# Kernel optimization log

Hardware: AMD Instinct MI355X
Metric: run time of the kernel (lower is better)

The kernel has to match this reference:

```python
import jax, jax.numpy as jnp
import numpy as np


def setup_inputs() -> dict:
    key = jax.random.key(0)
    kZ, kQ, kW, kU, kbk = jax.random.split(key, 5)
    B, E, D = 64, 16, 64
    N_ATOMS = 200000
    N_NP = 160000
    N_BK = 20000
    Q_DIM = 64
    Z = jax.random.normal(kZ, (B, E, D), dtype=jnp.float32)
    Q = jax.random.normal(kQ, (B, Q_DIM), dtype=jnp.float32)
    W = jax.random.normal(kW, (N_NP, D), dtype=jnp.float32)
    U = jax.random.normal(kU, (N_NP, Q_DIM), dtype=jnp.float32)
    np_indices = jnp.arange(N_NP, dtype=jnp.int64 if jax.config.jax_enable_x64 else jnp.int32)
    bk_indices = jax.random.randint(kbk, (N_BK,), 0, N_ATOMS, dtype=jnp.int32)
    return {"Z": Z, "Q": Q, "W": W, "U": U,
            "np_indices": np_indices, "bk_indices": bk_indices,
            "n_atoms": N_ATOMS}


def reference(Z, Q, W, U, np_indices, bk_indices, n_atoms):
    # Batched valuation for all neural-predicate atoms at once:
    # vm(Z, Q, atom_i) = sigmoid(sum_{e,d} Z[b,e,d] * W[i,d] + Q[b] . U[i])
    scores = jax.nn.sigmoid(jnp.einsum('bed,nd->bn', Z, W) + Q @ U.T)  # [B, n_np]
    B = Z.shape[0]
    V = jnp.zeros((B, n_atoms), dtype=jnp.float32)
    V = V.at[:, 0].set(1.0)                 # V[:, 0] = 1.0 (true atom)
    V = V.at[:, np_indices].set(scores)     # scatter valuation outputs
    V = V.at[:, bk_indices].add(1.0)        # background knowledge atoms += 1
    return V
```

## Files before the change

kernel.cpp:

```cpp
#include <hip/hip_runtime.h>


typedef _Float16 half8_t __attribute__((ext_vector_type(8)));
typedef float float4_t __attribute__((ext_vector_type(4)));

#define E_DIM 16
#define D_DIM 64
#define QD    64

__device__ inline half8_t pack8(float4_t lo, float4_t hi) {
    half8_t r;
    r[0] = (_Float16)lo[0]; r[1] = (_Float16)lo[1];
    r[2] = (_Float16)lo[2]; r[3] = (_Float16)lo[3];
    r[4] = (_Float16)hi[0]; r[5] = (_Float16)hi[1];
    r[6] = (_Float16)hi[2]; r[7] = (_Float16)hi[3];
    return r;
}

__global__ void prep_kernel(const float* __restrict__ Z, const float* __restrict__ Q,
                            const int* __restrict__ bk, int n_bk,
                            _Float16* __restrict__ Afrag, float* __restrict__ cnt) {
    int blk = blockIdx.x;
    int tid = threadIdx.x;
    if (blk < 32) {
        int t = blk * 256 + tid;
        int b = t >> 7, k = t & 127;
        float v;
        if (k < D_DIM) {
            const float* zp = Z + (size_t)b * E_DIM * D_DIM + k;
            v = 0.f;
            #pragma unroll
            for (int e = 0; e < E_DIM; ++e) v += zp[e * D_DIM];
        } else {
            v = Q[b * QD + (k - D_DIM)];
        }
        int mt = b >> 4, r = b & 15;
        int kq = k >> 5, j = k & 7, quad = (k >> 3) & 3;
        int lane = r + quad * 16;
        Afrag[(((mt * 4 + kq) * 64) + lane) * 8 + j] = (_Float16)v;
    } else if (cnt) {
        int i = (blk - 32) * 256 + tid;
        if (i < n_bk) atomicAdd(&cnt[bk[i]], 1.0f);
    }
}

__global__ __launch_bounds__(256) void main_kernel(
        const float* __restrict__ W, const float* __restrict__ U,
        const _Float16* __restrict__ Afrag, const float* __restrict__ cnt,
        float* __restrict__ V, int n_np, int n_atoms) {
    int tid = threadIdx.x;
    long long nblk = (long long)blockIdx.x * 64;

    if (nblk >= n_np) {
        int row = tid >> 2;
        long long c0 = nblk + (long long)(tid & 3) * 16;
        float4_t* vp = (float4_t*)(V + (size_t)row * n_atoms + c0);
        if (cnt) {
            const float4_t* cp = (const float4_t*)(cnt + c0);
            #pragma unroll
            for (int q = 0; q < 4; ++q) vp[q] = cp[q];
        } else {
            float4_t z = {0.f, 0.f, 0.f, 0.f};
            #pragma unroll
            for (int q = 0; q < 4; ++q) vp[q] = z;
        }
        return;
    }

    int wv = tid >> 6, lane = tid & 63;
    int quad = lane >> 4, l15 = lane & 15;
    long long n0 = nblk + wv * 16;

    const half8_t* Ap = (const half8_t*)Afrag;
    half8_t a[4][4];
    #pragma unroll
    for (int mt = 0; mt < 4; ++mt)
        #pragma unroll
        for (int kq = 0; kq < 4; ++kq)
            a[mt][kq] = Ap[(mt * 4 + kq) * 64 + lane];

    const float* Wr = W + (size_t)(n0 + l15) * D_DIM + quad * 8;
    const float* Ur = U + (size_t)(n0 + l15) * QD + quad * 8;
    float4_t w0 = *(const float4_t*)(Wr);
    float4_t w1 = *(const float4_t*)(Wr + 4);
    float4_t w2 = *(const float4_t*)(Wr + 32);
    float4_t w3 = *(const float4_t*)(Wr + 36);
    float4_t u0 = *(const float4_t*)(Ur);
    float4_t u1 = *(const float4_t*)(Ur + 4);
    float4_t u2 = *(const float4_t*)(Ur + 32);
    float4_t u3 = *(const float4_t*)(Ur + 36);
    half8_t b0 = pack8(w0, w1);
    half8_t b1 = pack8(w2, w3);
    half8_t b2 = pack8(u0, u1);
    half8_t b3 = pack8(u2, u3);

    float4_t acc[4] = {{0.f,0.f,0.f,0.f},{0.f,0.f,0.f,0.f},
                       {0.f,0.f,0.f,0.f},{0.f,0.f,0.f,0.f}};
    #pragma unroll
    for (int mt = 0; mt < 4; ++mt) {
        acc[mt] = __builtin_amdgcn_mfma_f32_16x16x32_f16(a[mt][0], b0, acc[mt], 0, 0, 0);
        acc[mt] = __builtin_amdgcn_mfma_f32_16x16x32_f16(a[mt][1], b1, acc[mt], 0, 0, 0);
        acc[mt] = __builtin_amdgcn_mfma_f32_16x16x32_f16(a[mt][2], b2, acc[mt], 0, 0, 0);
        acc[mt] = __builtin_amdgcn_mfma_f32_16x16x32_f16(a[mt][3], b3, acc[mt], 0, 0, 0);
    }

    float cn = cnt ? cnt[n0 + l15] : 0.f;
    #pragma unroll
    for (int mt = 0; mt < 4; ++mt) {
        #pragma unroll
        for (int r = 0; r < 4; ++r) {
            int row = mt * 16 + quad * 4 + r;
            float s = 1.0f / (1.0f + __expf(-acc[mt][r])) + cn;
            V[(size_t)row * n_atoms + n0 + l15] = s;
        }
    }
}

__global__ void bk_scatter(const int* __restrict__ bk, int n_bk,
                           float* __restrict__ V, int n_atoms) {
    int i = blockIdx.x * 256 + threadIdx.x;
    if (i < n_bk)
        atomicAdd(&V[(size_t)blockIdx.y * n_atoms + bk[i]], 1.0f);
}

extern "C" void kernel_launch(void* const* d_in, const int* in_sizes, int n_in,
                              void* d_out, int out_size, void* d_ws, size_t ws_size,
                              hipStream_t stream) {
    const float* Z = (const float*)d_in[0];
    const float* Q = (const float*)d_in[1];
    const float* W = (const float*)d_in[2];
    const float* U = (const float*)d_in[3];
    const int* bk = (const int*)d_in[5];
    float* V = (float*)d_out;

    int B       = in_sizes[0] / (E_DIM * D_DIM);
    int n_np    = in_sizes[2] / D_DIM;
    int n_bk    = in_sizes[5];
    int n_atoms = out_size / B;

    _Float16* Afrag = (_Float16*)d_ws;
    size_t need = 16384 + (size_t)n_atoms * sizeof(float);
    bool use_cnt = ws_size >= need;
    float* cnt = use_cnt ? (float*)((char*)d_ws + 16384) : nullptr;

    if (use_cnt) {
        hipMemsetAsync(cnt, 0, (size_t)n_atoms * sizeof(float), stream);
        int cnt_blocks = (n_bk + 255) / 256;
        prep_kernel<<<32 + cnt_blocks, 256, 0, stream>>>(Z, Q, bk, n_bk, Afrag, cnt);
    } else {
        prep_kernel<<<32, 256, 0, stream>>>(Z, Q, bk, n_bk, Afrag, nullptr);
    }

    int nb = n_atoms / 64;
    main_kernel<<<nb, 256, 0, stream>>>(W, U, Afrag, cnt, V, n_np, n_atoms);

    if (!use_cnt) {
        dim3 g((n_bk + 255) / 256, B);
        bk_scatter<<<g, 256, 0, stream>>>(bk, n_bk, V, n_atoms);
    }
}
```

Measured before the change: 142.0 us.

## Stage W/U through LDS and transpose outputs for vectorized coalesced stores

W and U tiles are now loaded cooperatively with fully coalesced float4 reads, converted to fp16 and staged in padded shared memory, and each wave then reads its MFMA B fragments from LDS. The accumulators are written transposed into shared memory so every thread can emit float4 stores along the atom dimension instead of scattered 4-byte stores. The tail blocks use the same float4 layout. This adds two extra barriers and LDS traffic in exchange for wider, better-coalesced global reads and writes of the large output matrix.

```diff
diff --git a/kernel.cpp b/kernel.cpp
--- a/kernel.cpp
+++ b/kernel.cpp
@@ -2,20 +2,12 @@
 
 
 typedef _Float16 half8_t __attribute__((ext_vector_type(8)));
+typedef _Float16 half4_t __attribute__((ext_vector_type(4)));
 typedef float float4_t __attribute__((ext_vector_type(4)));
 
 #define E_DIM 16
 #define D_DIM 64
 #define QD    64
-
-__device__ inline half8_t pack8(float4_t lo, float4_t hi) {
-    half8_t r;
-    r[0] = (_Float16)lo[0]; r[1] = (_Float16)lo[1];
-    r[2] = (_Float16)lo[2]; r[3] = (_Float16)lo[3];
-    r[4] = (_Float16)hi[0]; r[5] = (_Float16)hi[1];
-    r[6] = (_Float16)hi[2]; r[7] = (_Float16)hi[3];
-    return r;
-}
 
 __global__ void prep_kernel(const float* __restrict__ Z, const float* __restrict__ Q,
                             const int* __restrict__ bk, int n_bk,
@@ -44,32 +36,35 @@
     }
 }
 
+#define WH_STRIDE 72
+#define ET_STRIDE 68
+
 __global__ __launch_bounds__(256) void main_kernel(
         const float* __restrict__ W, const float* __restrict__ U,
         const _Float16* __restrict__ Afrag, const float* __restrict__ cnt,
         float* __restrict__ V, int n_np, int n_atoms) {
+    __shared__ __align__(16) char smem_raw[2 * 64 * WH_STRIDE * 2];
     int tid = threadIdx.x;
     long long nblk = (long long)blockIdx.x * 64;
+    int c  = tid & 15;
+    int rr = tid >> 4;
 
     if (nblk >= n_np) {
-        int row = tid >> 2;
-        long long c0 = nblk + (long long)(tid & 3) * 16;
-        float4_t* vp = (float4_t*)(V + (size_t)row * n_atoms + c0);
-        if (cnt) {
-            const float4_t* cp = (const float4_t*)(cnt + c0);
-            #pragma unroll
-            for (int q = 0; q < 4; ++q) vp[q] = cp[q];
-        } else {
-            float4_t z = {0.f, 0.f, 0.f, 0.f};
-            #pragma unroll
-            for (int q = 0; q < 4; ++q) vp[q] = z;
+        float4_t cn4 = {0.f, 0.f, 0.f, 0.f};
+        if (cnt) cn4 = *(const float4_t*)(cnt + nblk + 4 * c);
+        #pragma unroll
+        for (int p = 0; p < 4; ++p) {
+            int row = p * 16 + rr;
+            *(float4_t*)(V + (size_t)row * n_atoms + nblk + 4 * c) = cn4;
         }
         return;
     }
 
+    _Float16(*Wh)[WH_STRIDE] = (_Float16(*)[WH_STRIDE])smem_raw;
+    _Float16(*Uh)[WH_STRIDE] = (_Float16(*)[WH_STRIDE])(smem_raw + 64 * WH_STRIDE * 2);
+
     int wv = tid >> 6, lane = tid & 63;
     int quad = lane >> 4, l15 = lane & 15;
-    long long n0 = nblk + wv * 16;
 
     const half8_t* Ap = (const half8_t*)Afrag;
     half8_t a[4][4];
@@ -79,20 +74,26 @@
         for (int kq = 0; kq < 4; ++kq)
             a[mt][kq] = Ap[(mt * 4 + kq) * 64 + lane];
 
-    const float* Wr = W + (size_t)(n0 + l15) * D_DIM + quad * 8;
-    const float* Ur = U + (size_t)(n0 + l15) * QD + quad * 8;
-    float4_t w0 = *(const float4_t*)(Wr);
-    float4_t w1 = *(const float4_t*)(Wr + 4);
-    float4_t w2 = *(const float4_t*)(Wr + 32);
-    float4_t w3 = *(const float4_t*)(Wr + 36);
-    float4_t u0 = *(const float4_t*)(Ur);
-    float4_t u1 = *(const float4_t*)(Ur + 4);
-    float4_t u2 = *(const float4_t*)(Ur + 32);
-    float4_t u3 = *(const float4_t*)(Ur + 36);
-    half8_t b0 = pack8(w0, w1);
-    half8_t b1 = pack8(w2, w3);
-    half8_t b2 = pack8(u0, u1);
-    half8_t b3 = pack8(u2, u3);
+    const float4_t* Wg = (const float4_t*)(W + (size_t)nblk * D_DIM);
+    const float4_t* Ug = (const float4_t*)(U + (size_t)nblk * QD);
+    #pragma unroll
+    for (int i = 0; i < 4; ++i) {
+        int j = tid + i * 256;
+        int row = j >> 4, k = (j & 15) * 4;
+        float4_t w = Wg[j], u = Ug[j];
+        half4_t wh, uh;
+        #pragma unroll
+        for (int q = 0; q < 4; ++q) { wh[q] = (_Float16)w[q]; uh[q] = (_Float16)u[q]; }
+        *(half4_t*)&Wh[row][k] = wh;
+        *(half4_t*)&Uh[row][k] = uh;
+    }
+    __syncthreads();
+
+    int rB = wv * 16 + l15;
+    half8_t b0 = *(const half8_t*)&Wh[rB][quad * 8];
+    half8_t b1 = *(const half8_t*)&Wh[rB][32 + quad * 8];
+    half8_t b2 = *(const half8_t*)&Uh[rB][quad * 8];
+    half8_t b3 = *(const half8_t*)&Uh[rB][32 + quad * 8];
 
     float4_t acc[4] = {{0.f,0.f,0.f,0.f},{0.f,0.f,0.f,0.f},
                        {0.f,0.f,0.f,0.f},{0.f,0.f,0.f,0.f}};
@@ -104,15 +105,27 @@
         acc[mt] = __builtin_amdgcn_mfma_f32_16x16x32_f16(a[mt][3], b3, acc[mt], 0, 0, 0);
     }
 
-    float cn = cnt ? cnt[n0 + l15] : 0.f;
+    __syncthreads();
+    float(*eT)[ET_STRIDE] = (float(*)[ET_STRIDE])smem_raw;
+
     #pragma unroll
-    for (int mt = 0; mt < 4; ++mt) {
+    for (int mt = 0; mt < 4; ++mt)
         #pragma unroll
-        for (int r = 0; r < 4; ++r) {
-            int row = mt * 16 + quad * 4 + r;
-            float s = 1.0f / (1.0f + __expf(-acc[mt][r])) + cn;
-            V[(size_t)row * n_atoms + n0 + l15] = s;
-        }
+        for (int r = 0; r < 4; ++r)
+            eT[mt * 16 + quad * 4 + r][wv * 16 + l15] = acc[mt][r];
+    __syncthreads();
+
+    float4_t cn4 = {0.f, 0.f, 0.f, 0.f};
+    if (cnt) cn4 = *(const float4_t*)(cnt + nblk + 4 * c);
+    #pragma unroll
+    for (int p = 0; p < 4; ++p) {
+        int row = p * 16 + rr;
+        float4_t v = *(const float4_t*)&eT[row][4 * c];
+        float4_t s;
+        #pragma unroll
+        for (int q = 0; q < 4; ++q)
+            s[q] = 1.0f / (1.0f + __expf(-v[q])) + cn4[q];
+        *(float4_t*)(V + (size_t)row * n_atoms + nblk + 4 * c) = s;
     }
 }
 
```

Result: faster. 139.1 us (-2.0%).
